# Optimization experiments

Measured on AMD Instinct MI355X. Metric: run time of the kernel, lower is better.

## Reference

```python
import jax, jax.numpy as jnp
import numpy as np

B, N, D = 8, 4096, 512
H, R = 8, 256
DEPTH = D // H


def setup_inputs() -> dict:
    key = jax.random.key(0)
    ks = jax.random.split(key, 8)
    g = lambda k, shape, fan: jax.random.normal(k, shape, jnp.float32) * np.sqrt(2.0 / fan)
    return {
        "x": jax.random.normal(ks[0], (B, N, D), jnp.float32),
        "wq": g(ks[1], (D, D), 2 * D),
        "wk": g(ks[2], (D, D), 2 * D),
        "wv": g(ks[3], (D, D), 2 * D),
        "E": g(ks[4], (H, N, R), N + R),
        "F": g(ks[5], (H, N, R), N + R),
        "w_dense": g(ks[6], (D, D), 2 * D),
        "b_dense": jnp.zeros((D,), jnp.float32),
    }


def reference(x, wq, wk, wv, E, F, w_dense, b_dense):
    b = x.shape[0]
    split = lambda t: t.reshape(b, N, H, DEPTH).transpose(0, 2, 1, 3)  # -> bhnd
    q = split(x @ wq)
    k = split(x @ wk)
    v = split(x @ wv)
    # low-rank Linformer projections of K and V along sequence dim
    k_proj = jnp.einsum('bhnd,hnr->bhrd', k, E)
    v_proj = jnp.einsum('bhnd,hnr->bhrd', v, F)
    scores = jnp.einsum('bhnd,bhrd->bhnr', q, k_proj) / jnp.sqrt(jnp.float32(DEPTH))
    attn = jax.nn.softmax(scores, axis=-1)
    out = jnp.einsum('bhnr,bhrd->bhnd', attn, v_proj)
    concat = out.transpose(0, 2, 1, 3).reshape(b, N, D)
    return concat @ w_dense + b_dense
```

## Files before the change

kernel.cpp:

```cpp
#include <hip/hip_runtime.h>


typedef __bf16 bf16;
typedef __attribute__((ext_vector_type(8))) __bf16 bf16x8;
typedef __attribute__((ext_vector_type(8))) unsigned short ushort8;
typedef __attribute__((ext_vector_type(4))) float floatx4;

#define MFMA16(a, b, c) __builtin_amdgcn_mfma_f32_16x16x32_bf16((a), (b), (c), 0, 0, 0)

static __device__ __forceinline__ unsigned short bf_bits(float f) {
  unsigned u = __builtin_bit_cast(unsigned, f);
  u += 0x7fffu + ((u >> 16) & 1u);
  return (unsigned short)(u >> 16);
}
static __device__ __forceinline__ bf16 f2bf(float f) {
  unsigned short s = bf_bits(f);
  return __builtin_bit_cast(bf16, s);
}
static __device__ __forceinline__ float bf2f(bf16 v) {
  unsigned u = (unsigned)__builtin_bit_cast(unsigned short, v) << 16;
  return __builtin_bit_cast(float, u);
}
static __device__ __forceinline__ void async_copy16(const void* g, void* l) {
  __builtin_amdgcn_global_load_lds((const __attribute__((address_space(1))) void*)g,
                                   (__attribute__((address_space(3))) void*)l, 16, 0, 0);
}

__global__ void cvt_bf16_kernel(const float* __restrict__ src, bf16* __restrict__ dst) {
  long i = ((long)blockIdx.x * 256 + threadIdx.x) * 8;
  float4 a = *(const float4*)(src + i);
  float4 b = *(const float4*)(src + i + 4);
  ushort8 o;
  o[0] = bf_bits(a.x); o[1] = bf_bits(a.y); o[2] = bf_bits(a.z); o[3] = bf_bits(a.w);
  o[4] = bf_bits(b.x); o[5] = bf_bits(b.y); o[6] = bf_bits(b.z); o[7] = bf_bits(b.w);
  *(ushort8*)(dst + i) = o;
}

__global__ void transpose_w4_kernel(const float* __restrict__ wq, const float* __restrict__ wk,
                                    const float* __restrict__ wv, const float* __restrict__ wd,
                                    bf16* __restrict__ Wt, bf16* __restrict__ wdT) {
  const int z = blockIdx.z;
  const float* src = z == 0 ? wq : (z == 1 ? wk : (z == 2 ? wv : wd));
  bf16* dst = z < 3 ? Wt + (long)z * 262144 : wdT;
  __shared__ float tile[32][33];
  const int k0 = blockIdx.x * 32, n0 = blockIdx.y * 32;
  const int tx = threadIdx.x, ty = threadIdx.y;
#pragma unroll
  for (int i = ty; i < 32; i += 8)
    tile[i][tx] = src[(long)(k0 + i) * 512 + n0 + tx];
  __syncthreads();
#pragma unroll
  for (int i = ty; i < 32; i += 8)
    dst[(long)(n0 + i) * 512 + k0 + tx] = f2bf(tile[tx][i]);
}

__global__ void transpose_ef_kernel(const float* __restrict__ E, const float* __restrict__ F,
                                    bf16* __restrict__ Et, bf16* __restrict__ Ft) {
  const int z = blockIdx.z, h = z & 7;
  const float* src = (z < 8 ? E : F) + (long)h * 4096 * 256;
  bf16* dst = (z < 8 ? Et : Ft) + (long)h * 256 * 4096;
  __shared__ float tile[32][33];
  const int k0 = blockIdx.x * 32, n0 = blockIdx.y * 32;
  const int tx = threadIdx.x, ty = threadIdx.y;
#pragma unroll
  for (int i = ty; i < 32; i += 8)
    tile[i][tx] = src[(long)(k0 + i) * 256 + n0 + tx];
  __syncthreads();
#pragma unroll
  for (int i = ty; i < 32; i += 8)
    dst[(long)(n0 + i) * 4096 + k0 + tx] = f2bf(tile[tx][i]);
}

template <int MODE>
__global__ __launch_bounds__(256) void gemm128_kernel(
    const bf16* __restrict__ A, const bf16* __restrict__ Bt,
    bf16* __restrict__ oq, bf16* __restrict__ ok, bf16* __restrict__ ov,
    float* __restrict__ of, const float* __restrict__ bias) {
  constexpr int NB = MODE == 0 ? 12 : 4;
  const int lin = blockIdx.x;
  const int p = lin & 7, q = lin >> 3;
  const int m0 = (p * 32 + q / NB) * 128, n0 = (q % NB) * 128;
  __shared__ bf16 As[128][64];
  __shared__ bf16 Bs[128][64];
  const int t = threadIdx.x;
  const int w = t >> 6, l = t & 63, quad = l >> 4, lc = l & 15;
  const int wr = w >> 1, wc = w & 1;
  const int srow = w * 32 + (l >> 3);
  const int scol = (l & 7) * 8;
  const bf16* ga = A + (long)(m0 + srow) * 512 + scol;
  const bf16* gb = Bt + (long)(n0 + srow) * 512 + scol;
  floatx4 acc[4][4] = {};
  for (int k0 = 0; k0 < 512; k0 += 64) {
#pragma unroll
    for (int i = 0; i < 4; ++i) {
      async_copy16(ga + k0 + (long)i * 8 * 512, &As[w * 32 + i * 8][0]);
      async_copy16(gb + k0 + (long)i * 8 * 512, &Bs[w * 32 + i * 8][0]);
    }
    __syncthreads();
#pragma unroll
    for (int kk = 0; kk < 64; kk += 32) {
      bf16x8 af[4], bfr[4];
#pragma unroll
      for (int mt = 0; mt < 4; ++mt)
        af[mt] = *(const bf16x8*)&As[wr * 64 + mt * 16 + lc][kk + quad * 8];
#pragma unroll
      for (int nt = 0; nt < 4; ++nt)
        bfr[nt] = *(const bf16x8*)&Bs[wc * 64 + nt * 16 + lc][kk + quad * 8];
#pragma unroll
      for (int mt = 0; mt < 4; ++mt)
#pragma unroll
        for (int nt = 0; nt < 4; ++nt)
          acc[mt][nt] = MFMA16(af[mt], bfr[nt], acc[mt][nt]);
    }
    __syncthreads();
  }
  if (MODE == 0) {
    const int which = n0 >> 9, nb = n0 & 511;
    bf16* dst = which == 0 ? oq : (which == 1 ? ok : ov);
#pragma unroll
    for (int mt = 0; mt < 4; ++mt)
#pragma unroll
      for (int nt = 0; nt < 4; ++nt)
#pragma unroll
        for (int i = 0; i < 4; ++i) {
          int row = m0 + wr * 64 + mt * 16 + quad * 4 + i;
          int col = nb + wc * 64 + nt * 16 + lc;
          dst[(long)row * 512 + col] = f2bf(acc[mt][nt][i]);
        }
  } else {
#pragma unroll
    for (int mt = 0; mt < 4; ++mt)
#pragma unroll
      for (int nt = 0; nt < 4; ++nt)
#pragma unroll
        for (int i = 0; i < 4; ++i) {
          int row = m0 + wr * 64 + mt * 16 + quad * 4 + i;
          int col = n0 + wc * 64 + nt * 16 + lc;
          of[(long)row * 512 + col] = acc[mt][nt][i] + bias[col];
        }
  }
}

__global__ __launch_bounds__(256) void proj_kernel(
    const bf16* __restrict__ Et_g, const bf16* __restrict__ Ft_g,
    const bf16* __restrict__ kb, const bf16* __restrict__ vb,
    bf16* __restrict__ kp_part, bf16* __restrict__ vp_part) {
  const int z = blockIdx.z;
  const bf16* Big = z ? Ft_g : Et_g;
  const bf16* src = z ? vb : kb;
  bf16* out = z ? vp_part : kp_part;
  const int bh = blockIdx.y, b = bh >> 3, h = bh & 7;
  const int nbase = blockIdx.x * 1024;
  __shared__ bf16 Eb[256][64];
  __shared__ bf16 Kt[64][72];
  const int t = threadIdx.x;
  const int w = t >> 6, l = t & 63, quad = l >> 4, lc = l & 15;
  const int ecol = (l & 7) * 8;
  const bf16* gE = Big + ((long)h * 256 + w * 64 + (l >> 3)) * 4096 + nbase + ecol;
  const int sn = t >> 3, sq = t & 7;
  const bf16* gK = src + (long)(b * 4096 + nbase + sn) * 512 + h * 64 + sq * 8;
  floatx4 acc[4][4] = {};
  for (int ks = 0; ks < 16; ++ks) {
    bf16x8 kv0 = *(const bf16x8*)(gK + (long)(ks * 64) * 512);
    bf16x8 kv1 = *(const bf16x8*)(gK + (long)(ks * 64 + 32) * 512);
    __syncthreads();
#pragma unroll
    for (int i = 0; i < 8; ++i)
      async_copy16(gE + ks * 64 + (long)i * 8 * 4096, &Eb[w * 64 + i * 8][0]);
#pragma unroll
    for (int jj = 0; jj < 8; ++jj) Kt[sq * 8 + jj][sn ^ (sq * 8)] = kv0[jj];
#pragma unroll
    for (int jj = 0; jj < 8; ++jj) Kt[sq * 8 + jj][(32 + sn) ^ (sq * 8)] = kv1[jj];
    __syncthreads();
#pragma unroll
    for (int kk = 0; kk < 64; kk += 32) {
      bf16x8 af[4], bfr[4];
      if (z == 0) {
#pragma unroll
        for (int mt = 0; mt < 4; ++mt)
          af[mt] = *(const bf16x8*)&Eb[w * 64 + mt * 16 + lc][kk + quad * 8];
#pragma unroll
        for (int nt = 0; nt < 4; ++nt) {
          int d = nt * 16 + lc;
          bfr[nt] = *(const bf16x8*)&Kt[d][(kk + quad * 8) ^ ((d >> 3) << 3)];
        }
      } else {
#pragma unroll
        for (int mt = 0; mt < 4; ++mt) {
          int d = mt * 16 + lc;
          af[mt] = *(const bf16x8*)&Kt[d][(kk + quad * 8) ^ ((d >> 3) << 3)];
        }
#pragma unroll
        for (int nt = 0; nt < 4; ++nt)
          bfr[nt] = *(const bf16x8*)&Eb[w * 64 + nt * 16 + lc][kk + quad * 8];
      }
#pragma unroll
      for (int mt = 0; mt < 4; ++mt)
#pragma unroll
        for (int nt = 0; nt < 4; ++nt)
          acc[mt][nt] = MFMA16(af[mt], bfr[nt], acc[mt][nt]);
    }
  }
  bf16* obase = out + ((long)blockIdx.x * 64 + bh) * 16384;
  if (z == 0) {
#pragma unroll
    for (int mt = 0; mt < 4; ++mt)
#pragma unroll
      for (int nt = 0; nt < 4; ++nt)
#pragma unroll
        for (int i = 0; i < 4; ++i) {
          int r = w * 64 + mt * 16 + quad * 4 + i, d = nt * 16 + lc;
          obase[(long)r * 64 + d] = f2bf(acc[mt][nt][i]);
        }
  } else {
#pragma unroll
    for (int mt = 0; mt < 4; ++mt)
#pragma unroll
      for (int nt = 0; nt < 4; ++nt)
#pragma unroll
        for (int i = 0; i < 4; ++i) {
          int d = mt * 16 + quad * 4 + i, r = w * 64 + nt * 16 + lc;
          obase[(long)d * 256 + r] = f2bf(acc[mt][nt][i]);
        }
  }
}

__global__ __launch_bounds__(512) void attn_kernel(
    const bf16* __restrict__ qb, const bf16* __restrict__ kp_part,
    const bf16* __restrict__ vp_part, bf16* __restrict__ ao) {
  const int bx = blockIdx.x, h = blockIdx.y, b = blockIdx.z;
  const int bh = b * 8 + h;
  __shared__ __align__(16) char smem_u[36864];
  __shared__ bf16 Pc[2][128][40];
  bf16(*kpl)[72] = (bf16(*)[72])smem_u;
  bf16(*vtl)[264] = (bf16(*)[264])smem_u;
  const int t = threadIdx.x;
  const int w = t >> 6, l = t & 63, quad = l >> 4, lc = l & 15;

  {
    const bf16* p = kp_part + (long)bh * 16384;
#pragma unroll
    for (int j = 0; j < 4; ++j) {
      long e = (long)(j * 512 + t) * 8;
      bf16x8 a = *(const bf16x8*)(p + e);
      bf16x8 bb = *(const bf16x8*)(p + 1048576 + e);
      bf16x8 c = *(const bf16x8*)(p + 2097152 + e);
      bf16x8 d = *(const bf16x8*)(p + 3145728 + e);
      bf16x8 o;
#pragma unroll
      for (int jj = 0; jj < 8; ++jj)
        o[jj] = f2bf(bf2f(a[jj]) + bf2f(bb[jj]) + bf2f(c[jj]) + bf2f(d[jj]));
      int e32 = j * 512 + t;
      *(bf16x8*)&kpl[e32 >> 3][(e32 & 7) * 8] = o;
    }
  }
  __syncthreads();

  const long qrow = (long)(b * 4096 + bx * 128 + w * 16 + lc) * 512 + h * 64;
  floatx4 acc[16] = {};
#pragma unroll
  for (int kk = 0; kk < 64; kk += 32) {
    bf16x8 a = *(const bf16x8*)(qb + qrow + kk + quad * 8);
#pragma unroll
    for (int nt = 0; nt < 16; ++nt) {
      bf16x8 bfr = *(const bf16x8*)&kpl[nt * 16 + lc][kk + quad * 8];
      acc[nt] = MFMA16(a, bfr, acc[nt]);
    }
  }
  __syncthreads();

  {
    const bf16* p = vp_part + (long)bh * 16384;
#pragma unroll
    for (int j = 0; j < 4; ++j) {
      long e = (long)(j * 512 + t) * 8;
      bf16x8 a = *(const bf16x8*)(p + e);
      bf16x8 bb = *(const bf16x8*)(p + 1048576 + e);
      bf16x8 c = *(const bf16x8*)(p + 2097152 + e);
      bf16x8 d = *(const bf16x8*)(p + 3145728 + e);
      bf16x8 o;
#pragma unroll
      for (int jj = 0; jj < 8; ++jj)
        o[jj] = f2bf(bf2f(a[jj]) + bf2f(bb[jj]) + bf2f(c[jj]) + bf2f(d[jj]));
      int e32 = j * 512 + t;
      *(bf16x8*)&vtl[e32 >> 5][(e32 & 31) * 8] = o;
    }
  }

  float mx[4] = {-1e30f, -1e30f, -1e30f, -1e30f};
#pragma unroll
  for (int nt = 0; nt < 16; ++nt)
#pragma unroll
    for (int i = 0; i < 4; ++i) {
      acc[nt][i] *= 0.125f;
      mx[i] = fmaxf(mx[i], acc[nt][i]);
    }
#pragma unroll
  for (int m = 1; m <= 8; m <<= 1)
#pragma unroll
    for (int i = 0; i < 4; ++i) mx[i] = fmaxf(mx[i], __shfl_xor(mx[i], m, 64));
  float sm[4] = {0.f, 0.f, 0.f, 0.f};
#pragma unroll
  for (int nt = 0; nt < 16; ++nt)
#pragma unroll
    for (int i = 0; i < 4; ++i) {
      float pp = __expf(acc[nt][i] - mx[i]);
      acc[nt][i] = pp;
      sm[i] += pp;
    }
#pragma unroll
  for (int m = 1; m <= 8; m <<= 1)
#pragma unroll
    for (int i = 0; i < 4; ++i) sm[i] += __shfl_xor(sm[i], m, 64);
  float inv[4];
#pragma unroll
  for (int i = 0; i < 4; ++i) inv[i] = 1.0f / sm[i];

  floatx4 acc2[4] = {};
  for (int rs = 0; rs < 8; ++rs) {
    const int buf = rs & 1;
#pragma unroll
    for (int u = 0; u < 2; ++u) {
      int nt = rs * 2 + u;
#pragma unroll
      for (int i = 0; i < 4; ++i)
        Pc[buf][w * 16 + quad * 4 + i][u * 16 + lc] = f2bf(acc[nt][i] * inv[i]);
    }
    __syncthreads();
    bf16x8 a2 = *(const bf16x8*)&Pc[buf][w * 16 + lc][quad * 8];
#pragma unroll
    for (int nt = 0; nt < 4; ++nt) {
      bf16x8 b2 = *(const bf16x8*)&vtl[nt * 16 + lc][rs * 32 + quad * 8];
      acc2[nt] = MFMA16(a2, b2, acc2[nt]);
    }
  }

#pragma unroll
  for (int nt = 0; nt < 4; ++nt)
#pragma unroll
    for (int i = 0; i < 4; ++i) {
      int row = bx * 128 + w * 16 + quad * 4 + i;
      int d = nt * 16 + lc;
      ao[(long)(b * 4096 + row) * 512 + h * 64 + d] = f2bf(acc2[nt][i]);
    }
}

extern "C" void kernel_launch(void* const* d_in, const int* in_sizes, int n_in,
                              void* d_out, int out_size, void* d_ws, size_t ws_size,
                              hipStream_t stream) {
  const float* x  = (const float*)d_in[0];
  const float* wq = (const float*)d_in[1];
  const float* wk = (const float*)d_in[2];
  const float* wv = (const float*)d_in[3];
  const float* E  = (const float*)d_in[4];
  const float* F  = (const float*)d_in[5];
  const float* wd = (const float*)d_in[6];
  const float* bd = (const float*)d_in[7];
  float* out = (float*)d_out;

  char* ws = (char*)d_ws;
  bf16* x_bf    = (bf16*)(ws + 0);
  bf16* q_bf    = (bf16*)(ws + 33554432l);
  bf16* k_bf    = (bf16*)(ws + 67108864l);
  bf16* v_bf    = (bf16*)(ws + 100663296l);
  bf16* Et_g    = (bf16*)(ws + 134217728l);
  bf16* Ft_g    = (bf16*)(ws + 150994944l);
  bf16* Wt      = (bf16*)(ws + 167772160l);
  bf16* wdT     = (bf16*)(ws + 169345024l);
  bf16* kp_part = (bf16*)(ws + 169869312l);
  bf16* vp_part = (bf16*)(ws + 178257920l);
  bf16* attn_o  = x_bf;

  dim3 tb(32, 8);
  cvt_bf16_kernel<<<8192, 256, 0, stream>>>(x, x_bf);
  transpose_w4_kernel<<<dim3(16, 16, 4), tb, 0, stream>>>(wq, wk, wv, wd, Wt, wdT);
  transpose_ef_kernel<<<dim3(128, 8, 16), tb, 0, stream>>>(E, F, Et_g, Ft_g);

  gemm128_kernel<0><<<3072, 256, 0, stream>>>(x_bf, Wt, q_bf, k_bf, v_bf, nullptr, nullptr);
  proj_kernel<<<dim3(4, 64, 2), 256, 0, stream>>>(Et_g, Ft_g, k_bf, v_bf, kp_part, vp_part);
  attn_kernel<<<dim3(32, 8, 8), 512, 0, stream>>>(q_bf, kp_part, vp_part, attn_o);
  gemm128_kernel<1><<<1024, 256, 0, stream>>>(attn_o, wdT, nullptr, nullptr, nullptr, out, bd);
}
```

Before: 389.3 us.

## Replace 128x128 GEMMs with 256x256-tile 4-stage pipelined swizzled LDS GEMM

The QKV and output projection GEMMs move from 128x128 tiles with a single LDS buffer to 256x256 tiles run by 512 threads. Each k-step of 32 comes from a 4-deep ring of async global-to-LDS copies that are overlapped with the MFMAs through explicit vmcnt waits, setprio and an XOR-swizzled LDS layout to avoid bank conflicts. The aim is more data reuse per tile, hidden load latency and fewer barriers. In exchange it uses 128KB of dynamic shared memory and a larger accumulator set (128 floats per thread), and launches fewer blocks (256 for the output GEMM), which may leave CUs underfilled.

```diff
diff --git a/kernel.cpp b/kernel.cpp
--- a/kernel.cpp
+++ b/kernel.cpp
@@ -72,69 +72,115 @@
 }
 
 template <int MODE>
-__global__ __launch_bounds__(256) void gemm128_kernel(
+__global__ __launch_bounds__(512, 2) void gemm256_kernel(
     const bf16* __restrict__ A, const bf16* __restrict__ Bt,
     bf16* __restrict__ oq, bf16* __restrict__ ok, bf16* __restrict__ ov,
     float* __restrict__ of, const float* __restrict__ bias) {
-  constexpr int NB = MODE == 0 ? 12 : 4;
+  constexpr int NBt = MODE == 0 ? 6 : 2;
+  extern __shared__ __align__(16) char smem[];
   const int lin = blockIdx.x;
   const int p = lin & 7, q = lin >> 3;
-  const int m0 = (p * 32 + q / NB) * 128, n0 = (q % NB) * 128;
-  __shared__ bf16 As[128][64];
-  __shared__ bf16 Bs[128][64];
+  const int m0 = (p * 16 + q / NBt) * 256, n0 = (q % NBt) * 256;
   const int t = threadIdx.x;
   const int w = t >> 6, l = t & 63, quad = l >> 4, lc = l & 15;
-  const int wr = w >> 1, wc = w & 1;
-  const int srow = w * 32 + (l >> 3);
-  const int scol = (l & 7) * 8;
-  const bf16* ga = A + (long)(m0 + srow) * 512 + scol;
-  const bf16* gb = Bt + (long)(n0 + srow) * 512 + scol;
-  floatx4 acc[4][4] = {};
-  for (int k0 = 0; k0 < 512; k0 += 64) {
-#pragma unroll
-    for (int i = 0; i < 4; ++i) {
-      async_copy16(ga + k0 + (long)i * 8 * 512, &As[w * 32 + i * 8][0]);
-      async_copy16(gb + k0 + (long)i * 8 * 512, &Bs[w * 32 + i * 8][0]);
-    }
-    __syncthreads();
-#pragma unroll
-    for (int kk = 0; kk < 64; kk += 32) {
-      bf16x8 af[4], bfr[4];
-#pragma unroll
-      for (int mt = 0; mt < 4; ++mt)
-        af[mt] = *(const bf16x8*)&As[wr * 64 + mt * 16 + lc][kk + quad * 8];
-#pragma unroll
-      for (int nt = 0; nt < 4; ++nt)
-        bfr[nt] = *(const bf16x8*)&Bs[wc * 64 + nt * 16 + lc][kk + quad * 8];
-#pragma unroll
-      for (int mt = 0; mt < 4; ++mt)
-#pragma unroll
-        for (int nt = 0; nt < 4; ++nt)
-          acc[mt][nt] = MFMA16(af[mt], bfr[nt], acc[mt][nt]);
-    }
-    __syncthreads();
-  }
+  const int wr = w >> 2, wc = w & 3;
+
+  const int srow = w * 16 + (l >> 2);
+  const int sq = (l & 3) ^ ((l >> 3) & 3);
+  const bf16* gA0 = A + (long)(m0 + srow) * 512 + sq * 8;
+  const bf16* gB0 = Bt + (long)(n0 + srow) * 512 + sq * 8;
+  bf16* AsW = (bf16*)smem + w * 512;
+  bf16* BsW = (bf16*)(smem + 65536) + w * 512;
+
+  const int swz = (quad ^ ((lc >> 1) & 3)) << 4;
+  const int a_rd = (wr * 128 + lc) * 64 + swz;
+  const int b_rd = (wc * 64 + lc) * 64 + swz;
+
+  floatx4 acc[8][4] = {};
+
+#define STAGE_A(s_, buf_)                                              \
+  do {                                                                 \
+    async_copy16(gA0 + (s_) * 32, AsW + (buf_) * 8192);                \
+    async_copy16(gA0 + 65536l + (s_) * 32, AsW + (buf_) * 8192 + 4096);\
+  } while (0)
+#define STAGE_B(s_, buf_)                                              \
+  do {                                                                 \
+    async_copy16(gB0 + (s_) * 32, BsW + (buf_) * 8192);                \
+    async_copy16(gB0 + 65536l + (s_) * 32, BsW + (buf_) * 8192 + 4096);\
+  } while (0)
+
+  STAGE_A(0, 0); STAGE_B(0, 0);
+  STAGE_A(1, 1); STAGE_B(1, 1);
+  STAGE_A(2, 2); STAGE_B(2, 2);
+  asm volatile("s_waitcnt vmcnt(8)" ::: "memory");
+  __builtin_amdgcn_sched_barrier(0);
+  __builtin_amdgcn_s_barrier();
+  __builtin_amdgcn_sched_barrier(0);
+
+#pragma unroll
+  for (int s = 0; s < 16; ++s) {
+    const int buf = s & 3, tb = (s + 3) & 3;
+    const char* Ab = smem + buf * 16384;
+    const char* Bb = smem + 65536 + buf * 16384;
+    bf16x8 af[4], bfr[4];
+#pragma unroll
+    for (int nt = 0; nt < 4; ++nt)
+      bfr[nt] = *(const bf16x8*)(Bb + b_rd + nt * 1024);
+#pragma unroll
+    for (int mt = 0; mt < 4; ++mt)
+      af[mt] = *(const bf16x8*)(Ab + a_rd + mt * 1024);
+    if (s < 13) STAGE_A(s + 3, tb);
+    __builtin_amdgcn_s_setprio(1);
+#pragma unroll
+    for (int mt = 0; mt < 4; ++mt)
+#pragma unroll
+      for (int nt = 0; nt < 4; ++nt)
+        acc[mt][nt] = MFMA16(af[mt], bfr[nt], acc[mt][nt]);
+    __builtin_amdgcn_s_setprio(0);
+#pragma unroll
+    for (int mt = 0; mt < 4; ++mt)
+      af[mt] = *(const bf16x8*)(Ab + a_rd + (mt + 4) * 1024);
+    if (s < 13) STAGE_B(s + 3, tb);
+    __builtin_amdgcn_s_setprio(1);
+#pragma unroll
+    for (int mt = 0; mt < 4; ++mt)
+#pragma unroll
+      for (int nt = 0; nt < 4; ++nt)
+        acc[mt + 4][nt] = MFMA16(af[mt], bfr[nt], acc[mt + 4][nt]);
+    __builtin_amdgcn_s_setprio(0);
+    if (s < 15) {
+      if (s <= 12)      { asm volatile("s_waitcnt vmcnt(8)" ::: "memory"); }
+      else if (s == 13) { asm volatile("s_waitcnt vmcnt(4)" ::: "memory"); }
+      else              { asm volatile("s_waitcnt vmcnt(0)" ::: "memory"); }
+      __builtin_amdgcn_sched_barrier(0);
+      __builtin_amdgcn_s_barrier();
+      __builtin_amdgcn_sched_barrier(0);
+    }
+  }
+#undef STAGE_A
+#undef STAGE_B
+
   if (MODE == 0) {
     const int which = n0 >> 9, nb = n0 & 511;
     bf16* dst = which == 0 ? oq : (which == 1 ? ok : ov);
 #pragma unroll
-    for (int mt = 0; mt < 4; ++mt)
+    for (int mt = 0; mt < 8; ++mt)
 #pragma unroll
       for (int nt = 0; nt < 4; ++nt)
 #pragma unroll
         for (int i = 0; i < 4; ++i) {
-          int row = m0 + wr * 64 + mt * 16 + quad * 4 + i;
+          int row = m0 + wr * 128 + mt * 16 + quad * 4 + i;
           int col = nb + wc * 64 + nt * 16 + lc;
           dst[(long)row * 512 + col] = f2bf(acc[mt][nt][i]);
         }
   } else {
 #pragma unroll
-    for (int mt = 0; mt < 4; ++mt)
+    for (int mt = 0; mt < 8; ++mt)
 #pragma unroll
       for (int nt = 0; nt < 4; ++nt)
 #pragma unroll
         for (int i = 0; i < 4; ++i) {
-          int row = m0 + wr * 64 + mt * 16 + quad * 4 + i;
+          int row = m0 + wr * 128 + mt * 16 + quad * 4 + i;
           int col = n0 + wc * 64 + nt * 16 + lc;
           of[(long)row * 512 + col] = acc[mt][nt][i] + bias[col];
         }
@@ -371,13 +417,22 @@
   bf16* vp_part = (bf16*)(ws + 178257920l);
   bf16* attn_o  = x_bf;
 
+  static bool attr_done = false;
+  if (!attr_done) {
+    hipFuncSetAttribute((const void*)gemm256_kernel<0>,
+                        hipFuncAttributeMaxDynamicSharedMemorySize, 131072);
+    hipFuncSetAttribute((const void*)gemm256_kernel<1>,
+                        hipFuncAttributeMaxDynamicSharedMemorySize, 131072);
+    attr_done = true;
+  }
+
   dim3 tb(32, 8);
   cvt_bf16_kernel<<<8192, 256, 0, stream>>>(x, x_bf);
   transpose_w4_kernel<<<dim3(16, 16, 4), tb, 0, stream>>>(wq, wk, wv, wd, Wt, wdT);
   transpose_ef_kernel<<<dim3(128, 8, 16), tb, 0, stream>>>(E, F, Et_g, Ft_g);
 
-  gemm128_kernel<0><<<3072, 256, 0, stream>>>(x_bf, Wt, q_bf, k_bf, v_bf, nullptr, nullptr);
+  gemm256_kernel<0><<<768, 512, 131072, stream>>>(x_bf, Wt, q_bf, k_bf, v_bf, nullptr, nullptr);
   proj_kernel<<<dim3(4, 64, 2), 256, 0, stream>>>(Et_g, Ft_g, k_bf, v_bf, kp_part, vp_part);
   attn_kernel<<<dim3(32, 8, 8), 512, 0, stream>>>(q_bf, kp_part, vp_part, attn_o);
-  gemm128_kernel<1><<<1024, 256, 0, stream>>>(attn_o, wdT, nullptr, nullptr, nullptr, out, bd);
-}
+  gemm256_kernel<1><<<256, 512, 131072, stream>>>(attn_o, wdT, nullptr, nullptr, nullptr, out, bd);
+}
```

Measured after the change: 381.6 us. 2.0% less time.
